# Kernel tuning notes

Hardware: AMD Instinct MI355X
Metric: run time of the kernel (lower is better)

## Reference

```python
import jax, jax.numpy as jnp
import numpy as np

B, N, C = 4, 2048, 1024
H = 16
D = C // H

def setup_inputs() -> dict:
    key = jax.random.key(0)
    k1, k2, k3 = jax.random.split(key, 3)
    x = jax.random.normal(k1, (B, N, C), dtype=jnp.float32)
    qkv_w = jax.random.normal(k2, (3 * C, C), dtype=jnp.float32) * (1.0 / np.sqrt(C))
    qkv_b = jax.random.normal(k3, (3 * C,), dtype=jnp.float32) * 0.02
    return {"x": x, "qkv_w": qkv_w, "qkv_b": qkv_b}

def reference(x, qkv_w, qkv_b):
    b, n, c = x.shape
    # torch Linear: x @ W^T + b
    qkv = x @ qkv_w.T + qkv_b                      # [B,N,3C]
    qkv = qkv.reshape(b, n, 3, H, D)
    qkv = jnp.transpose(qkv, (2, 0, 3, 1, 4))       # [3,B,H,N,D]
    q, k, v = qkv[0], qkv[1], qkv[2]
    attn = jnp.einsum('bhnd,bhmd->bhnm', q, k) / jnp.sqrt(jnp.asarray(D, x.dtype))
    attn = jax.nn.softmax(attn, axis=-1)
    out = jnp.einsum('bhnm,bhmd->bhnd', attn, v)    # [B,H,N,D]
    out = jnp.transpose(out, (0, 2, 1, 3)).reshape(b, n, c)
    return out
```

## Files before the change

kernel.cpp:

```cpp
#include <hip/hip_runtime.h>
#include <hip/hip_bf16.h>

typedef __attribute__((ext_vector_type(8))) short short8;
typedef __attribute__((ext_vector_type(4))) float f32x4;
typedef __attribute__((ext_vector_type(4))) unsigned int u32x4;
typedef unsigned short u16;
typedef unsigned int u32;

typedef u32 __attribute__((address_space(1))) as1_u32;
typedef u32 __attribute__((address_space(3))) as3_u32;

#define NB 4
#define SEQ 2048
#define CH 1024
#define NH 16
#define HD 64
#define M_TOT (NB*SEQ)
#define N_TOT (3*CH)
#define K_TOT CH
#define SCL 0.18033688f

#define MFMA16(a,b,c) __builtin_amdgcn_mfma_f32_16x16x32_bf16((a),(b),(c),0,0,0)

__device__ __forceinline__ u16 f2bf(float f) {
    union { float f; u32 u; } v; v.f = f;
    u32 u = v.u;
    return (u16)((u + 0x7fffu + ((u >> 16) & 1u)) >> 16);
}

__device__ __forceinline__ u32 pkbf2(float a, float b) {
    union { __hip_bfloat162 h; u32 u; } x;
    x.h = __float22bfloat162_rn(float2{a, b});
    return x.u;
}

__global__ void cvt_bf16_kernel(const float* __restrict__ src, u16* __restrict__ dst, int n8) {
    int i = blockIdx.x * 256 + threadIdx.x;
    if (i >= n8) return;
    const float4* s4 = (const float4*)src;
    float4 a = s4[2*i], b = s4[2*i+1];
    u32x4 r;
    r[0] = pkbf2(a.x, a.y); r[1] = pkbf2(a.z, a.w);
    r[2] = pkbf2(b.x, b.y); r[3] = pkbf2(b.z, b.w);
    *(u32x4*)(dst + (size_t)i*8) = r;
}

__global__ __launch_bounds__(256) void qkv_gemm_kernel(
        const u16* __restrict__ A, const u16* __restrict__ W,
        const float* __restrict__ bias,
        u16* __restrict__ qw, u16* __restrict__ kw, u16* __restrict__ vtw)
{
    __shared__ u16 As[128*32];
    __shared__ u16 Bs[128*32];
    const int t = threadIdx.x;
    const int wave = t >> 6;
    const int lane = t & 63;
    const int l15 = lane & 15, lhi = lane >> 4;
    const int wr = wave >> 1, wc = wave & 1;
    const int bm = blockIdx.x, bn = blockIdx.y;

    f32x4 acc[4][4] = {};

    const int arow = t >> 2;
    const int acol = (t & 3) * 8;
    const u16* gA = A + (size_t)(bm*128 + arow)*K_TOT + acol;
    const u16* gB = W + (size_t)(bn*128 + arow)*K_TOT + acol;

    for (int k0 = 0; k0 < K_TOT; k0 += 32) {
        #pragma unroll
        for (int i = 0; i < 2; ++i) {
            __builtin_amdgcn_global_load_lds(
                (const as1_u32*)(gA + (size_t)i*64*K_TOT + k0),
                (as3_u32*)(As + i*2048 + wave*512), 16, 0, 0);
            __builtin_amdgcn_global_load_lds(
                (const as1_u32*)(gB + (size_t)i*64*K_TOT + k0),
                (as3_u32*)(Bs + i*2048 + wave*512), 16, 0, 0);
        }
        __syncthreads();
        short8 af[4], bfr[4];
        #pragma unroll
        for (int m = 0; m < 4; ++m)
            af[m] = *(const short8*)(As + (wr*64 + m*16 + l15)*32 + lhi*8);
        #pragma unroll
        for (int n = 0; n < 4; ++n)
            bfr[n] = *(const short8*)(Bs + (wc*64 + n*16 + l15)*32 + lhi*8);
        #pragma unroll
        for (int m = 0; m < 4; ++m)
            #pragma unroll
            for (int n = 0; n < 4; ++n)
                acc[m][n] = MFMA16(af[m], bfr[n], acc[m][n]);
        __syncthreads();
    }

    const int colbase = bn*128 + wc*64;
    const int which = colbase >> 10;
    float bv[4]; int hh[4], dd[4];
    #pragma unroll
    for (int n = 0; n < 4; ++n) {
        int cg = colbase + n*16 + l15;
        bv[n] = bias[cg];
        int hd = cg & 1023;
        hh[n] = hd >> 6; dd[n] = hd & 63;
    }
    #pragma unroll
    for (int m = 0; m < 4; ++m) {
        int rowg = bm*128 + wr*64 + m*16 + lhi*4;
        #pragma unroll
        for (int j = 0; j < 4; ++j) {
            int rg = rowg + j;
            int b = rg >> 11, nseq = rg & 2047;
            #pragma unroll
            for (int n = 0; n < 4; ++n) {
                float val = acc[m][n][j] + bv[n];
                size_t bhn = (size_t)(b*NH + hh[n]);
                if (which == 0) {
                    qw[(bhn*SEQ + nseq)*HD + dd[n]] = f2bf(val * SCL);
                } else if (which == 1) {
                    kw[(bhn*SEQ + nseq)*HD + dd[n]] = f2bf(val);
                } else {
                    int nl = nseq & 63, base = nseq & ~63;
                    int g = nl >> 5, kk = nl & 31, sub = kk >> 4, low = kk & 15;
                    int pos = g*32 + low*2 + sub;
                    vtw[(bhn*HD + dd[n])*SEQ + base + pos] = f2bf(val);
                }
            }
        }
    }
}

__global__ __launch_bounds__(512) void attn_kernel(
        const u16* __restrict__ qw, const u16* __restrict__ kw,
        const u16* __restrict__ vtw, float* __restrict__ out)
{
    __shared__ u16 Ksh[2][64*64];
    __shared__ u16 Vsh[2][64*64];
    __shared__ u16 P[8][32*72];
    const int t = threadIdx.x;
    const int wave = t >> 6, lane = t & 63;
    const int l15 = lane & 15, lhi = lane >> 4;
    const int bh = blockIdx.y;
    const int b = bh >> 4, h = bh & 15;
    const int q0 = blockIdx.x * 256 + wave * 32;

    const u16* Q  = qw  + (size_t)bh * SEQ * HD;
    const u16* Kg = kw  + (size_t)bh * SEQ * HD;
    const u16* Vg = vtw + (size_t)bh * HD * SEQ;

    const int srow = lane >> 3;
    const int scol = ((lane & 7) ^ srow) * 8;
    const int crow = wave * 8 + srow;

    auto STAGE = [&](int buf, int kv) {
        __builtin_amdgcn_global_load_lds(
            (const as1_u32*)(Kg + (size_t)(kv + crow)*HD + scol),
            (as3_u32*)(&Ksh[buf][wave*8*64]), 16, 0, 0);
        __builtin_amdgcn_global_load_lds(
            (const as1_u32*)(Vg + (size_t)crow*SEQ + kv + scol),
            (as3_u32*)(&Vsh[buf][wave*8*64]), 16, 0, 0);
    };

    STAGE(0, 0);

    short8 qf[2][2];
    #pragma unroll
    for (int rf = 0; rf < 2; ++rf)
        #pragma unroll
        for (int ks = 0; ks < 2; ++ks)
            qf[rf][ks] = *(const short8*)(Q + (size_t)(q0 + rf*16 + l15)*HD + ks*32 + lhi*8);

    f32x4 o[2][4] = {};
    float lpart[2][4] = {};

    __syncthreads();

    int cur = 0;
    for (int kv0 = 0; kv0 < SEQ; kv0 += 64) {
        if (kv0 + 64 < SEQ) STAGE(cur ^ 1, kv0 + 64);

        f32x4 s[2][4] = {};
        #pragma unroll
        for (int ks = 0; ks < 2; ++ks)
            #pragma unroll
            for (int n = 0; n < 4; ++n) {
                int lr = n*16 + l15;
                short8 kf = *(const short8*)(&Ksh[cur][lr*64 + ((ks*32 + lhi*8) ^ ((l15 & 7)*8))]);
                s[0][n] = MFMA16(qf[0][ks], kf, s[0][n]);
                s[1][n] = MFMA16(qf[1][ks], kf, s[1][n]);
            }

        #pragma unroll
        for (int rf = 0; rf < 2; ++rf) {
            #pragma unroll
            for (int j = 0; j < 4; ++j) {
                float p0 = __builtin_amdgcn_exp2f(s[rf][0][j]);
                float p1 = __builtin_amdgcn_exp2f(s[rf][1][j]);
                float p2 = __builtin_amdgcn_exp2f(s[rf][2][j]);
                float p3 = __builtin_amdgcn_exp2f(s[rf][3][j]);
                lpart[rf][j] += (p0 + p1) + (p2 + p3);
                int prow = rf*16 + lhi*4 + j;
                *(u32*)&P[wave][prow*72 +      2*l15] = pkbf2(p0, p1);
                *(u32*)&P[wave][prow*72 + 32 + 2*l15] = pkbf2(p2, p3);
            }
        }
        asm volatile("s_waitcnt lgkmcnt(0)" ::: "memory");

        #pragma unroll
        for (int ks = 0; ks < 2; ++ks) {
            short8 pa0 = *(const short8*)(&P[wave][(     l15)*72 + ks*32 + lhi*8]);
            short8 pa1 = *(const short8*)(&P[wave][(16 + l15)*72 + ks*32 + lhi*8]);
            #pragma unroll
            for (int nd = 0; nd < 4; ++nd) {
                int lr = nd*16 + l15;
                short8 vf = *(const short8*)(&Vsh[cur][lr*64 + ((ks*32 + lhi*8) ^ ((l15 & 7)*8))]);
                o[0][nd] = MFMA16(pa0, vf, o[0][nd]);
                o[1][nd] = MFMA16(pa1, vf, o[1][nd]);
            }
        }
        __syncthreads();
        cur ^= 1;
    }

    #pragma unroll
    for (int rf = 0; rf < 2; ++rf)
        #pragma unroll
        for (int j = 0; j < 4; ++j) {
            float l = lpart[rf][j];
            l += __shfl_xor(l, 1);
            l += __shfl_xor(l, 2);
            l += __shfl_xor(l, 4);
            l += __shfl_xor(l, 8);
            float inv = 1.0f / l;
            int qrow = q0 + rf*16 + lhi*4 + j;
            float* orow = out + ((size_t)(b*SEQ + qrow))*CH + h*HD;
            #pragma unroll
            for (int nd = 0; nd < 4; ++nd)
                orow[nd*16 + l15] = o[rf][nd][j] * inv;
        }
}

extern "C" void kernel_launch(void* const* d_in, const int* in_sizes, int n_in,
                              void* d_out, int out_size, void* d_ws, size_t ws_size,
                              hipStream_t stream) {
    const float* x    = (const float*)d_in[0];
    const float* w    = (const float*)d_in[1];
    const float* bias = (const float*)d_in[2];
    float* out = (float*)d_out;

    const size_t BHND = (size_t)NB*NH*SEQ*HD;
    u16* qw  = (u16*)d_ws;
    u16* kw  = qw  + BHND;
    u16* vtw = kw  + BHND;
    u16* xbf = vtw + BHND;
    u16* wbf = xbf + (size_t)M_TOT*K_TOT;

    int nx8 = M_TOT*K_TOT/8;
    int nw8 = N_TOT*K_TOT/8;
    cvt_bf16_kernel<<<nx8/256, 256, 0, stream>>>(x, xbf, nx8);
    cvt_bf16_kernel<<<nw8/256, 256, 0, stream>>>(w, wbf, nw8);
    qkv_gemm_kernel<<<dim3(M_TOT/128, N_TOT/128), 256, 0, stream>>>(xbf, wbf, bias, qw, kw, vtw);
    attn_kernel<<<dim3(SEQ/256, NB*NH), 512, 0, stream>>>(qw, kw, vtw, out);
}
```

Before: 179.2 us.

## Compute transposed S so P stays in registers, dropping LDS round trip

The QK^T MFMA now computes the transposed score tile (K as A operand), so each lane's accumulator already holds the probabilities it needs as the A operand of the PV MFMA. The P shared-memory buffer, its writes and the lgkmcnt wait go away. The K rows are permuted at staging time and the V transpose-permute in the projection is dropped so the register layout lines up. The row-sum reduction becomes a cross-group shuffle, and launch bounds now request 4 blocks per CU, which may constrain registers.

```diff
diff --git a/kernel.cpp b/kernel.cpp
--- a/kernel.cpp
+++ b/kernel.cpp
@@ -118,23 +118,19 @@
                 } else if (which == 1) {
                     kw[(bhn*SEQ + nseq)*HD + dd[n]] = f2bf(val);
                 } else {
-                    int nl = nseq & 63, base = nseq & ~63;
-                    int g = nl >> 5, kk = nl & 31, sub = kk >> 4, low = kk & 15;
-                    int pos = g*32 + low*2 + sub;
-                    vtw[(bhn*HD + dd[n])*SEQ + base + pos] = f2bf(val);
+                    vtw[(bhn*HD + dd[n])*SEQ + nseq] = f2bf(val);
                 }
             }
         }
     }
 }
 
-__global__ __launch_bounds__(512) void attn_kernel(
+__global__ __launch_bounds__(512, 4) void attn_kernel(
         const u16* __restrict__ qw, const u16* __restrict__ kw,
         const u16* __restrict__ vtw, float* __restrict__ out)
 {
     __shared__ u16 Ksh[2][64*64];
     __shared__ u16 Vsh[2][64*64];
-    __shared__ u16 P[8][32*72];
     const int t = threadIdx.x;
     const int wave = t >> 6, lane = t & 63;
     const int l15 = lane & 15, lhi = lane >> 4;
@@ -149,10 +145,12 @@
     const int srow = lane >> 3;
     const int scol = ((lane & 7) ^ srow) * 8;
     const int crow = wave * 8 + srow;
+    const int kperm = (crow & 32) | ((crow & 12) << 1)
+                    | ((crow & 16) >> 2) | (crow & 3);
 
     auto STAGE = [&](int buf, int kv) {
         __builtin_amdgcn_global_load_lds(
-            (const as1_u32*)(Kg + (size_t)(kv + crow)*HD + scol),
+            (const as1_u32*)(Kg + (size_t)(kv + kperm)*HD + scol),
             (as3_u32*)(&Ksh[buf][wave*8*64]), 16, 0, 0);
         __builtin_amdgcn_global_load_lds(
             (const as1_u32*)(Vg + (size_t)crow*SEQ + kv + scol),
@@ -169,7 +167,7 @@
             qf[rf][ks] = *(const short8*)(Q + (size_t)(q0 + rf*16 + l15)*HD + ks*32 + lhi*8);
 
     f32x4 o[2][4] = {};
-    float lpart[2][4] = {};
+    float lpart[2] = {0.f, 0.f};
 
     __syncthreads();
 
@@ -177,41 +175,37 @@
     for (int kv0 = 0; kv0 < SEQ; kv0 += 64) {
         if (kv0 + 64 < SEQ) STAGE(cur ^ 1, kv0 + 64);
 
-        f32x4 s[2][4] = {};
-        #pragma unroll
-        for (int ks = 0; ks < 2; ++ks)
-            #pragma unroll
-            for (int n = 0; n < 4; ++n) {
-                int lr = n*16 + l15;
-                short8 kf = *(const short8*)(&Ksh[cur][lr*64 + ((ks*32 + lhi*8) ^ ((l15 & 7)*8))]);
-                s[0][n] = MFMA16(qf[0][ks], kf, s[0][n]);
-                s[1][n] = MFMA16(qf[1][ks], kf, s[1][n]);
-            }
-
-        #pragma unroll
-        for (int rf = 0; rf < 2; ++rf) {
-            #pragma unroll
-            for (int j = 0; j < 4; ++j) {
-                float p0 = __builtin_amdgcn_exp2f(s[rf][0][j]);
-                float p1 = __builtin_amdgcn_exp2f(s[rf][1][j]);
-                float p2 = __builtin_amdgcn_exp2f(s[rf][2][j]);
-                float p3 = __builtin_amdgcn_exp2f(s[rf][3][j]);
-                lpart[rf][j] += (p0 + p1) + (p2 + p3);
-                int prow = rf*16 + lhi*4 + j;
-                *(u32*)&P[wave][prow*72 +      2*l15] = pkbf2(p0, p1);
-                *(u32*)&P[wave][prow*72 + 32 + 2*l15] = pkbf2(p2, p3);
-            }
-        }
-        asm volatile("s_waitcnt lgkmcnt(0)" ::: "memory");
+        f32x4 st[2][4] = {};
+        #pragma unroll
+        for (int g = 0; g < 4; ++g)
+            #pragma unroll
+            for (int ks = 0; ks < 2; ++ks) {
+                short8 kf = *(const short8*)(&Ksh[cur][(g*16 + l15)*64 + ((ks*32 + lhi*8) ^ ((l15 & 7)*8))]);
+                st[0][g] = MFMA16(kf, qf[0][ks], st[0][g]);
+                st[1][g] = MFMA16(kf, qf[1][ks], st[1][g]);
+            }
+
+        u32x4 pa[2][2];
+        #pragma unroll
+        for (int rf = 0; rf < 2; ++rf)
+            #pragma unroll
+            for (int g = 0; g < 4; ++g) {
+                float p0 = __builtin_amdgcn_exp2f(st[rf][g][0]);
+                float p1 = __builtin_amdgcn_exp2f(st[rf][g][1]);
+                float p2 = __builtin_amdgcn_exp2f(st[rf][g][2]);
+                float p3 = __builtin_amdgcn_exp2f(st[rf][g][3]);
+                lpart[rf] += (p0 + p1) + (p2 + p3);
+                pa[rf][g >> 1][(g & 1)*2]     = pkbf2(p0, p1);
+                pa[rf][g >> 1][(g & 1)*2 + 1] = pkbf2(p2, p3);
+            }
 
         #pragma unroll
         for (int ks = 0; ks < 2; ++ks) {
-            short8 pa0 = *(const short8*)(&P[wave][(     l15)*72 + ks*32 + lhi*8]);
-            short8 pa1 = *(const short8*)(&P[wave][(16 + l15)*72 + ks*32 + lhi*8]);
+            short8 pa0 = __builtin_bit_cast(short8, pa[0][ks]);
+            short8 pa1 = __builtin_bit_cast(short8, pa[1][ks]);
             #pragma unroll
             for (int nd = 0; nd < 4; ++nd) {
-                int lr = nd*16 + l15;
-                short8 vf = *(const short8*)(&Vsh[cur][lr*64 + ((ks*32 + lhi*8) ^ ((l15 & 7)*8))]);
+                short8 vf = *(const short8*)(&Vsh[cur][(nd*16 + l15)*64 + ((ks*32 + lhi*8) ^ ((l15 & 7)*8))]);
                 o[0][nd] = MFMA16(pa0, vf, o[0][nd]);
                 o[1][nd] = MFMA16(pa1, vf, o[1][nd]);
             }
@@ -221,21 +215,20 @@
     }
 
     #pragma unroll
-    for (int rf = 0; rf < 2; ++rf)
+    for (int rf = 0; rf < 2; ++rf) {
+        float l = lpart[rf];
+        l += __shfl_xor(l, 16);
+        l += __shfl_xor(l, 32);
         #pragma unroll
         for (int j = 0; j < 4; ++j) {
-            float l = lpart[rf][j];
-            l += __shfl_xor(l, 1);
-            l += __shfl_xor(l, 2);
-            l += __shfl_xor(l, 4);
-            l += __shfl_xor(l, 8);
-            float inv = 1.0f / l;
+            float inv = 1.0f / __shfl(l, lhi*4 + j);
             int qrow = q0 + rf*16 + lhi*4 + j;
             float* orow = out + ((size_t)(b*SEQ + qrow))*CH + h*HD;
             #pragma unroll
             for (int nd = 0; nd < 4; ++nd)
                 orow[nd*16 + l15] = o[rf][nd][j] * inv;
         }
+    }
 }
 
 extern "C" void kernel_launch(void* const* d_in, const int* in_sizes, int n_in,
```

After: 176.1 us. No clear change (-1.7%).
